# Kernel tuning notes

Hardware: AMD Instinct MI355X
Metric: run time of the kernel (lower is better)

Reference implementation:

```python
import jax, jax.numpy as jnp
import numpy as np

EPS = 1e-4
RES_BALANCE = 0.3
ATTN_BALANCE = 0.3
CLIP_ACT = 256.0
NUM_HEADS = 4
CPH = 64  # channels_per_head


def normalize(x, axes):
    # EDM2 normalize: x / (eps + ||x||_axes / sqrt(prod(axes sizes)))  -> unit RMS
    axes = tuple(axes)
    n = jnp.sqrt(jnp.sum(jnp.square(x), axis=axes, keepdims=True))
    alpha = 1.0 / np.sqrt(float(np.prod([x.shape[a] for a in axes])))
    return x / (EPS + alpha * n)


def mp_silu(x):
    return jax.nn.silu(x) / 0.596


def mp_sum(a, b, t):
    return (a + t * (b - a)) / np.sqrt((1.0 - t) ** 2 + t ** 2)


def mp_conv2d(x, w, gain=1.0):
    # MPConv: forced weight normalization per output channel, then gain/sqrt(fan_in)
    fan_in = w.shape[1] * w.shape[2] * w.shape[3]
    w = normalize(w, (1, 2, 3)) * (gain / np.sqrt(float(fan_in)))
    pad = w.shape[-1] // 2
    return jax.lax.conv_general_dilated(
        x, w, window_strides=(1, 1), padding=[(pad, pad), (pad, pad)],
        dimension_numbers=('NCHW', 'OIHW', 'NCHW'))


def mp_linear(x, w, gain=1.0):
    fan_in = w.shape[1]
    w = normalize(w, (1,)) * (gain / np.sqrt(float(fan_in)))
    return x @ w.T


def setup_inputs() -> dict:
    key = jax.random.key(0)
    ks = jax.random.split(key, 8)
    N, Cin, Cout, Cemb, H, W = 32, 256, 256, 768, 32, 32
    return {
        'x': jax.random.normal(ks[0], (N, Cin, H, W), dtype=jnp.float32),
        'emb': jax.random.normal(ks[1], (N, Cemb), dtype=jnp.float32),
        'w_res0': jax.random.normal(ks[2], (Cout, Cout, 3, 3), dtype=jnp.float32),
        'w_emb': jax.random.normal(ks[3], (Cout, Cemb), dtype=jnp.float32),
        'w_res1': jax.random.normal(ks[4], (Cout, Cout, 3, 3), dtype=jnp.float32),
        'w_qkv': jax.random.normal(ks[5], (Cout * 3, Cout, 1, 1), dtype=jnp.float32),
        'w_proj': jax.random.normal(ks[6], (Cout, Cout, 1, 1), dtype=jnp.float32),
        'emb_gain': jax.random.normal(ks[7], (), dtype=jnp.float32),
    }


def reference(x, emb, w_res0, w_emb, w_res1, w_qkv, w_proj, emb_gain):
    N, C, H, W = x.shape
    S = H * W
    # flavor == 'enc', in_channels == out_channels -> no conv_skip; resample 'keep' is identity
    x = normalize(x, (1,))  # pixel norm over channels
    y = mp_conv2d(mp_silu(x), w_res0)
    c = mp_linear(emb, w_emb, gain=emb_gain) + 1.0  # [N, C]
    y = mp_silu(y * c[:, :, None, None])
    y = mp_conv2d(y, w_res1)
    x = mp_sum(x, y, RES_BALANCE)
    # QK-normalized self-attention over H*W tokens
    y = mp_conv2d(x, w_qkv)                              # [N, 3C, H, W]
    y = y.reshape(N, NUM_HEADS, CPH, 3, S)               # channel layout (h, c, qkv)
    y = normalize(y, (2,))                               # L2-normalize per head-channel vector
    q, k, v = y[:, :, :, 0], y[:, :, :, 1], y[:, :, :, 2]  # [N, h, c, S]
    logits = jnp.einsum('nhcq,nhck->nhqk', q, k) / np.sqrt(float(CPH))
    w_att = jax.nn.softmax(logits, axis=3)
    y = jnp.einsum('nhqk,nhck->nhcq', w_att, v).reshape(N, C, H, W)
    y = mp_conv2d(y, w_proj)
    x = mp_sum(x, y, ATTN_BALANCE)
    return jnp.clip(x, -CLIP_ACT, CLIP_ACT)
```

## Files before the change

### kernel.cpp

```cpp
#include <hip/hip_runtime.h>
#include <hip/hip_bf16.h>
#include <math.h>

#define EPSV 1e-4f
#define WA 0.91914503f
#define WB 0.39392215f
#define INV596 1.6778523f

typedef __bf16 bf16x8 __attribute__((ext_vector_type(8)));
typedef short  s16x8  __attribute__((ext_vector_type(8)));
typedef float  f32x4  __attribute__((ext_vector_type(4)));
typedef _Float16 f16x8 __attribute__((ext_vector_type(8)));

__device__ inline bf16x8 bzero8() { s16x8 z = 0; return __builtin_bit_cast(bf16x8, z); }

__device__ inline void store_bf4(__hip_bfloat16* p, float a, float b, float c, float d) {
    __hip_bfloat16 t[4];
    t[0] = __float2bfloat16(a); t[1] = __float2bfloat16(b);
    t[2] = __float2bfloat16(c); t[3] = __float2bfloat16(d);
    *(short4*)p = *(short4*)t;
}

__device__ inline float bfbits2f(short u) {
    return __uint_as_float(((unsigned)(unsigned short)u) << 16);
}

__global__ __launch_bounds__(256) void wnorm_all(
        const float* __restrict__ w_res0, const float* __restrict__ w_res1,
        const float* __restrict__ w_qkv, const float* __restrict__ w_proj,
        const float* __restrict__ w_emb, const float* __restrict__ emb_gain,
        __hip_bfloat16* __restrict__ W0B, __hip_bfloat16* __restrict__ W1B,
        __hip_bfloat16* __restrict__ WQB, __hip_bfloat16* __restrict__ WPB,
        float* __restrict__ WEN) {
    __shared__ float sdata[4];
    int b = blockIdx.x;
    int tid = threadIdx.x;
    int wid = tid >> 6, lane = tid & 63;

    if (b < 512) {
        int oc = b & 255;
        const float* row = ((b < 256) ? w_res0 : w_res1) + (size_t)oc * 2304;
        __hip_bfloat16* wb = (b < 256) ? W0B : W1B;
        float ss = 0.f;
        for (int i = tid; i < 2304; i += 256) { float v = row[i]; ss += v * v; }
#pragma unroll
        for (int m = 32; m >= 1; m >>= 1) ss += __shfl_xor(ss, m);
        if (lane == 0) sdata[wid] = ss;
        __syncthreads();
        float tot = sdata[0] + sdata[1] + sdata[2] + sdata[3];
        float s = (1.0f / 48.0f) / (EPSV + sqrtf(tot) * (1.0f / 48.0f));
        for (int i = tid; i < 2304; i += 256) {
            int ic = i / 9, tap = i - ic * 9;
            wb[((size_t)tap * 256 + oc) * 256 + ic] = __float2bfloat16(row[i] * s);
        }
    } else if (b < 1536) {
        bool isq = (b < 1280);
        int oc = isq ? (b - 512) : (b - 1280);
        const float* row = (isq ? w_qkv : w_proj) + (size_t)oc * 256;
        float v0 = row[tid];
        float ss = v0 * v0;
#pragma unroll
        for (int m = 32; m >= 1; m >>= 1) ss += __shfl_xor(ss, m);
        if (lane == 0) sdata[wid] = ss;
        __syncthreads();
        float tot = sdata[0] + sdata[1] + sdata[2] + sdata[3];
        float s = 0.0625f / (EPSV + sqrtf(tot) * 0.0625f);
        if (isq) {
            int h = oc / 192, rem = oc - h * 192;
            int c = rem / 3, t = rem - c * 3;
            int newoc = t * 256 + h * 64 + c;
            WQB[(size_t)newoc * 256 + tid] = __float2bfloat16(v0 * s);
        } else {
            WPB[(size_t)oc * 256 + tid] = __float2bfloat16(v0 * s);
        }
    } else {
        int r = b - 1536;
        const float* row = w_emb + (size_t)r * 768;
        float ss = 0.f;
        for (int i = tid; i < 768; i += 256) { float v = row[i]; ss += v * v; }
#pragma unroll
        for (int m = 32; m >= 1; m >>= 1) ss += __shfl_xor(ss, m);
        if (lane == 0) sdata[wid] = ss;
        __syncthreads();
        float tot = sdata[0] + sdata[1] + sdata[2] + sdata[3];
        float g = emb_gain[0];
        float s = g * 0.036084392f / (EPSV + sqrtf(tot) * 0.036084392f);
        float* outr = WEN + (size_t)r * 768;
        for (int i = tid; i < 768; i += 256) outr[i] = row[i] * s;
    }
}

__global__ __launch_bounds__(256) void pixnorm2(const float* __restrict__ x,
        float* __restrict__ Xn, __hip_bfloat16* __restrict__ Ah) {
    int n = blockIdx.y;
    int sp = blockIdx.x * 32 + (threadIdx.x & 31);
    int cg = threadIdx.x >> 5;
    const float* xb = x + (size_t)n * 262144 + ((size_t)cg << 15) + sp;
    float v[32];
    float ss = 0.f;
#pragma unroll
    for (int i = 0; i < 32; i++) {
        v[i] = xb[(size_t)i << 10];
        ss += v[i] * v[i];
    }
    __shared__ float red[8][33];
    red[cg][threadIdx.x & 31] = ss;
    __syncthreads();
    float tot = 0.f;
#pragma unroll
    for (int j = 0; j < 8; j++) tot += red[j][threadIdx.x & 31];
    float inv = 1.0f / (EPSV + sqrtf(tot) * 0.0625f);
    float* xo = Xn + ((size_t)n * 1024 + sp) * 256 + cg * 32;
    __hip_bfloat16* ao = Ah + ((size_t)n * 1024 + sp) * 256 + cg * 32;
#pragma unroll
    for (int i = 0; i < 32; i += 4) {
        float a0 = v[i] * inv, a1 = v[i+1] * inv, a2 = v[i+2] * inv, a3 = v[i+3] * inv;
        *(float4*)&xo[i] = make_float4(a0, a1, a2, a3);
        float s0 = a0 / (1.0f + __expf(-a0)) * INV596;
        float s1 = a1 / (1.0f + __expf(-a1)) * INV596;
        float s2 = a2 / (1.0f + __expf(-a2)) * INV596;
        float s3 = a3 / (1.0f + __expf(-a3)) * INV596;
        store_bf4(&ao[i], s0, s1, s2, s3);
    }
}

__global__ void emb_kernel(const float* __restrict__ emb, const float* __restrict__ wn,
                           float* __restrict__ cvec) {
    int n = blockIdx.x;
    __shared__ float es[768];
    for (int i = threadIdx.x; i < 768; i += 256) es[i] = emb[n * 768 + i];
    __syncthreads();
    const float* wr = wn + (size_t)threadIdx.x * 768;
    float acc = 0.f;
    for (int k = 0; k < 768; k++) acc += es[k] * wr[k];
    cvec[n * 256 + threadIdx.x] = acc + 1.0f;
}

template<int KS, int ORI, int EPI, int GX>
__global__ __launch_bounds__(256) void convmfma(
        const __hip_bfloat16* __restrict__ xin,
        const __hip_bfloat16* __restrict__ wb,
        __hip_bfloat16* __restrict__ out_h,
        float* __restrict__ out_f,
        const float* __restrict__ xres,
        __hip_bfloat16* __restrict__ out_h2,
        const float* __restrict__ cvec,
        int Cin, int Cout) {
    constexpr int TAPS = KS * KS;
    constexpr int RRD = 8 + KS - 1;
    constexpr int CCD = 32 + KS - 1;
    constexpr int HLO = KS / 2;
    constexpr int NX = (RRD * 128) / 256;
    __shared__ __align__(16) __hip_bfloat16 Xl[RRD * CCD * 32];
    __shared__ __align__(16) __hip_bfloat16 Wl[TAPS * 64 * 32];

    auto xoff = [](int rr, int cc, int gran) {
        int rowl = rr * CCD + cc;
        return rowl * 32 + ((gran ^ ((rowl >> 1) & 3)) << 3);
    };
    auto woff = [](int tap, int oc, int gran) {
        int rowl = tap * 64 + oc;
        return rowl * 32 + ((gran ^ ((rowl >> 1) & 3)) << 3);
    };

    int lin = blockIdx.x + GX * (blockIdx.y + 4 * blockIdx.z);
    constexpr int NBLK = GX * 4 * 32;
    constexpr int CPX = NBLK >> 3;
    int swz = (lin & 7) * CPX + (lin >> 3);
    int oc0 = (swz % GX) * 64;
    int W = swz / GX;
    int spblk = W & 3;
    int n = W >> 2;

    int tid = threadIdx.x;
    int r0 = spblk * 8;
    int lane = tid & 63, wv = tid >> 6;
    int l15 = lane & 15, g = lane >> 4;

    if (KS == 3) {
        if (tid < RRD * 2 * 4) {
            int rr = tid >> 3;
            int side = (tid >> 2) & 1;
            int slot = tid & 3;
            *(bf16x8*)&Xl[xoff(rr, side ? (CCD - 1) : 0, slot)] = bzero8();
        }
    }

    bf16x8 xp[NX];
    bf16x8 wpf[TAPS];
    auto loadX = [&](int ch) {
#pragma unroll
        for (int u = 0; u < NX; u++) {
            int f = tid + u * 256;
            int rr = f >> 7, rem = f & 127;
            int cc = rem >> 2, slot = rem & 3;
            int gr = r0 + rr - HLO;
            bf16x8 v = bzero8();
            if ((unsigned)gr < 32u)
                v = *(const bf16x8*)&xin[((size_t)n * 1024 + gr * 32 + cc) * Cin + ch * 32 + slot * 8];
            xp[u] = v;
        }
    };
    auto writeX = [&]() {
#pragma unroll
        for (int u = 0; u < NX; u++) {
            int f = tid + u * 256;
            int rr = f >> 7, rem = f & 127;
            int cc = rem >> 2, slot = rem & 3;
            *(bf16x8*)&Xl[xoff(rr, cc + HLO, slot)] = xp[u];
        }
    };
    auto loadW = [&](int ch) {
#pragma unroll
        for (int u = 0; u < TAPS; u++) {
            int f = tid + u * 256;
            int tap = f >> 8, rem = f & 255;
            int oc = rem >> 2, slot = rem & 3;
            wpf[u] = *(const bf16x8*)&wb[((size_t)tap * Cout + oc0 + oc) * Cin + ch * 32 + slot * 8];
        }
    };
    auto writeW = [&]() {
#pragma unroll
        for (int u = 0; u < TAPS; u++) {
            int f = tid + u * 256;
            int tap = f >> 8, rem = f & 255;
            int oc = rem >> 2, slot = rem & 3;
            *(bf16x8*)&Wl[woff(tap, oc, slot)] = wpf[u];
        }
    };

    f32x4 acc[4][4];
    const f32x4 z4 = {0.f, 0.f, 0.f, 0.f};
#pragma unroll
    for (int a = 0; a < 4; a++)
#pragma unroll
        for (int b = 0; b < 4; b++) acc[a][b] = z4;

    int nch = Cin >> 5;
    loadX(0); loadW(0);
    writeX(); writeW();
    __syncthreads();

    for (int ch = 0; ch < nch; ++ch) {
        bool pf = (ch + 1 < nch);
        if (pf) { loadX(ch + 1); loadW(ch + 1); }
        if constexpr (KS == 3) {
#pragma unroll
            for (int dx = 0; dx < 3; dx++) {
                bf16x8 xv[4][2];
#pragma unroll
                for (int r = 0; r < 4; r++)
#pragma unroll
                    for (int b = 0; b < 2; b++)
                        xv[r][b] = *(const bf16x8*)&Xl[xoff(2 * wv + r, b * 16 + l15 + dx, g)];
#pragma unroll
                for (int dy = 0; dy < 3; dy++) {
                    int tap = dy * 3 + dx;
                    bf16x8 af[4];
#pragma unroll
                    for (int of = 0; of < 4; of++)
                        af[of] = *(const bf16x8*)&Wl[woff(tap, of * 16 + l15, g)];
#pragma unroll
                    for (int of = 0; of < 4; of++)
#pragma unroll
                        for (int sf = 0; sf < 4; sf++) {
                            if (ORI == 1)
                                acc[of][sf] = __builtin_amdgcn_mfma_f32_16x16x32_bf16(af[of], xv[(sf >> 1) + dy][sf & 1], acc[of][sf], 0, 0, 0);
                            else
                                acc[of][sf] = __builtin_amdgcn_mfma_f32_16x16x32_bf16(xv[(sf >> 1) + dy][sf & 1], af[of], acc[of][sf], 0, 0, 0);
                        }
                }
            }
        } else {
#pragma unroll
            for (int tap = 0; tap < TAPS; ++tap) {
                bf16x8 af[4], bfv[4];
#pragma unroll
                for (int of = 0; of < 4; of++)
                    af[of] = *(const bf16x8*)&Wl[woff(tap, of * 16 + l15, g)];
#pragma unroll
                for (int sf = 0; sf < 4; sf++) {
                    int rr = 2 * wv + (sf >> 1);
                    int cc2 = (sf & 1) * 16 + l15;
                    bfv[sf] = *(const bf16x8*)&Xl[xoff(rr, cc2, g)];
                }
#pragma unroll
                for (int of = 0; of < 4; of++)
#pragma unroll
                    for (int sf = 0; sf < 4; sf++) {
                        if (ORI == 1)
                            acc[of][sf] = __builtin_amdgcn_mfma_f32_16x16x32_bf16(af[of], bfv[sf], acc[of][sf], 0, 0, 0);
                        else
                            acc[of][sf] = __builtin_amdgcn_mfma_f32_16x16x32_bf16(bfv[sf], af[of], acc[of][sf], 0, 0, 0);
                    }
            }
        }
        __syncthreads();
        if (pf) { writeX(); writeW(); __syncthreads(); }
    }

#pragma unroll
    for (int of = 0; of < 4; of++)
#pragma unroll
        for (int sf = 0; sf < 4; sf++) {
            if constexpr (ORI == 1) {
                int row_l = 2 * wv + (sf >> 1);
                int col = (sf & 1) * 16 + l15;
                int sp = spblk * 256 + row_l * 32 + col;
                int ocb = oc0 + of * 16 + (lane >> 4) * 4;
                size_t a = ((size_t)n * 1024 + sp) * Cout + ocb;
                if constexpr (EPI == 1) {
                    float vv[4];
#pragma unroll
                    for (int r = 0; r < 4; r++) {
                        float t = acc[of][sf][r] * cvec[n * 256 + ocb + r];
                        vv[r] = t / (1.0f + __expf(-t)) * INV596;
                    }
                    store_bf4(&out_h[a], vv[0], vv[1], vv[2], vv[3]);
                } else if constexpr (EPI == 2) {
                    float4 xr = *(const float4*)&xres[a];
                    float v0 = WA * xr.x + WB * acc[of][sf][0];
                    float v1 = WA * xr.y + WB * acc[of][sf][1];
                    float v2 = WA * xr.z + WB * acc[of][sf][2];
                    float v3 = WA * xr.w + WB * acc[of][sf][3];
                    *(float4*)&out_f[a] = make_float4(v0, v1, v2, v3);
                    store_bf4(&out_h2[a], v0, v1, v2, v3);
                } else {
                    store_bf4(&out_h[a], acc[of][sf][0], acc[of][sf][1],
                              acc[of][sf][2], acc[of][sf][3]);
                }
            } else {
                int oc = oc0 + of * 16 + l15;
                int spb = spblk * 256 + (2 * wv + (sf >> 1)) * 32 + (sf & 1) * 16 + (lane >> 4) * 4;
                if constexpr (EPI == 6) {
                    float vv[4];
#pragma unroll
                    for (int r = 0; r < 4; r++) {
                        float xr = xres[((size_t)n * 1024 + spb + r) * 256 + oc];
                        float vo = WA * xr + WB * acc[of][sf][r];
                        vv[r] = fminf(fmaxf(vo, -256.f), 256.f);
                    }
                    *(float4*)&out_f[((size_t)n * 256 + oc) * 1024 + spb] =
                        make_float4(vv[0], vv[1], vv[2], vv[3]);
                }
            }
        }
}

__global__ __launch_bounds__(192) void qkvnorm3(__hip_bfloat16* __restrict__ qkv3,
                                                _Float16* __restrict__ vt) {
    int n = blockIdx.y;
    int s0 = blockIdx.x * 16;
    int tid = threadIdx.x;
    int sl = tid / 12;
    int grp = tid - sl * 12;
    int t = grp >> 2, h = grp & 3;
    __hip_bfloat16* base = qkv3 + ((size_t)(n * 1024 + s0 + sl)) * 768 + t * 256 + h * 64;
    float v[64];
    float ss = 0.f;
#pragma unroll
    for (int j = 0; j < 8; j++) {
        s16x8 b = *(const s16x8*)(base + j * 8);
#pragma unroll
        for (int e = 0; e < 8; e++) {
            float f = bfbits2f(b[e]);
            v[j * 8 + e] = f; ss += f * f;
        }
    }
    float inv = 1.0f / (EPSV + sqrtf(ss) * 0.125f);
    if (t == 0) inv *= 0.18033688f;
    __shared__ _Float16 Ts[4][64][16];
    if (t < 2) {
#pragma unroll
        for (int j = 0; j < 8; j++) {
            _Float16 tmp[8];
#pragma unroll
            for (int e = 0; e < 8; e++) tmp[e] = (_Float16)(v[j * 8 + e] * inv);
            *(s16x8*)(base + j * 8) = *(s16x8*)tmp;
        }
    } else {
#pragma unroll
        for (int c = 0; c < 64; c++) Ts[h][c][sl] = (_Float16)(v[c] * inv);
    }
    __syncthreads();
    for (int i = tid; i < 256; i += 192) {
        int hh = i >> 6, c = i & 63;
        f16x8 w0 = *(const f16x8*)&Ts[hh][c][0];
        f16x8 w1 = *(const f16x8*)&Ts[hh][c][8];
        _Float16* dst = vt + ((size_t)((n * 4 + hh) * 64 + c)) * 1024 + s0;
        *(f16x8*)dst = w0;
        *(f16x8*)(dst + 8) = w1;
    }
}

__device__ inline int swz64(int row, int c8) { return row * 64 + ((c8 ^ (row & 7)) << 3); }

__global__ __launch_bounds__(512) void attn_mfma(const _Float16* __restrict__ qkv3,
                                                 const _Float16* __restrict__ vt,
                                                 __hip_bfloat16* __restrict__ outp) {
    int lin = blockIdx.x + 4 * (blockIdx.y + 4 * blockIdx.z);
    int swz = (lin & 7) * 64 + (lin >> 3);
    int qt = swz & 3;
    int W = swz >> 2;
    int h = W & 3, n = W >> 2;

    __shared__ __align__(16) _Float16 Ks[2][64 * 64];
    __shared__ __align__(16) _Float16 Vs[2][64 * 64];
    __shared__ __align__(16) _Float16 Ps[8][32 * 64];
    int tid = threadIdx.x;
    int lane = tid & 63, wv = tid >> 6;
    int l15 = lane & 15, g = lane >> 4;

    f16x8 qreg[2][2];
#pragma unroll
    for (int nf = 0; nf < 2; nf++)
#pragma unroll
        for (int cc = 0; cc < 2; cc++)
            qreg[nf][cc] = *(const f16x8*)&qkv3[
                ((size_t)(n * 1024 + qt * 256 + wv * 32 + nf * 16 + l15)) * 768 + h * 64 + cc * 32 + g * 8];

    f16x8 kp, vp;
    int krow = tid >> 3, kslot = tid & 7;
    auto loadKV = [&](int kt) {
        kp = *(const f16x8*)&qkv3[((size_t)(n * 1024 + kt * 64 + krow)) * 768 + 256 + h * 64 + kslot * 8];
        vp = *(const f16x8*)&vt[((size_t)((n * 4 + h) * 64 + krow)) * 1024 + kt * 64 + kslot * 8];
    };
    int kdst = swz64(krow, kslot);
    auto writeKV = [&](int b) {
        *(f16x8*)&Ks[b][kdst] = kp;
        *(f16x8*)&Vs[b][kdst] = vp;
    };

    f32x4 acc_o[2][4];
    const f32x4 z4 = {0.f, 0.f, 0.f, 0.f};
#pragma unroll
    for (int a = 0; a < 2; a++)
#pragma unroll
        for (int b = 0; b < 4; b++) acc_o[a][b] = z4;
    float l_run[2] = {0.f, 0.f};

    loadKV(0); writeKV(0);
    __syncthreads();

    for (int kt = 0; kt < 16; kt++) {
        int cur = kt & 1;
        if (kt < 15) loadKV(kt + 1);

        f32x4 accs[4][2];
#pragma unroll
        for (int a = 0; a < 4; a++)
#pragma unroll
            for (int b = 0; b < 2; b++) accs[a][b] = z4;
        __builtin_amdgcn_s_setprio(1);
#pragma unroll
        for (int cc = 0; cc < 2; cc++) {
            f16x8 kf[4];
#pragma unroll
            for (int mf = 0; mf < 4; mf++)
                kf[mf] = *(const f16x8*)&Ks[cur][swz64(mf * 16 + l15, cc * 4 + g)];
#pragma unroll
            for (int mf = 0; mf < 4; mf++)
#pragma unroll
                for (int nf = 0; nf < 2; nf++)
                    accs[mf][nf] = __builtin_amdgcn_mfma_f32_16x16x32_f16(kf[mf], qreg[nf][cc], accs[mf][nf], 0, 0, 0);
        }
        __builtin_amdgcn_s_setprio(0);

#pragma unroll
        for (int nf = 0; nf < 2; nf++) {
            int q = nf * 16 + l15;
            float rs = 0.f;
#pragma unroll
            for (int mf = 0; mf < 4; mf++) {
                float p0 = __builtin_amdgcn_exp2f(accs[mf][nf][0]);
                float p1 = __builtin_amdgcn_exp2f(accs[mf][nf][1]);
                float p2 = __builtin_amdgcn_exp2f(accs[mf][nf][2]);
                float p3 = __builtin_amdgcn_exp2f(accs[mf][nf][3]);
                rs += (p0 + p1) + (p2 + p3);
                unsigned w0 = __builtin_bit_cast(unsigned, __builtin_amdgcn_cvt_pkrtz(p0, p1));
                unsigned w1 = __builtin_bit_cast(unsigned, __builtin_amdgcn_cvt_pkrtz(p2, p3));
                int elem = swz64(q, mf * 2 + (g >> 1)) + (g & 1) * 4;
                *(uint2*)&Ps[wv][elem] = make_uint2(w0, w1);
            }
            l_run[nf] += rs;
        }

        __builtin_amdgcn_s_setprio(1);
#pragma unroll
        for (int kc = 0; kc < 2; kc++) {
            f16x8 pf[2], vf[4];
#pragma unroll
            for (int mf2 = 0; mf2 < 2; mf2++)
                pf[mf2] = *(const f16x8*)&Ps[wv][swz64(mf2 * 16 + l15, kc * 4 + g)];
#pragma unroll
            for (int nf2 = 0; nf2 < 4; nf2++)
                vf[nf2] = *(const f16x8*)&Vs[cur][swz64(nf2 * 16 + l15, kc * 4 + g)];
#pragma unroll
            for (int mf2 = 0; mf2 < 2; mf2++)
#pragma unroll
                for (int nf2 = 0; nf2 < 4; nf2++)
                    acc_o[mf2][nf2] = __builtin_amdgcn_mfma_f32_16x16x32_f16(pf[mf2], vf[nf2], acc_o[mf2][nf2], 0, 0, 0);
        }
        __builtin_amdgcn_s_setprio(0);

        if (kt < 15) writeKV(cur ^ 1);
        __syncthreads();
    }

#pragma unroll
    for (int nf = 0; nf < 2; nf++) {
        float l = l_run[nf];
        l += __shfl_xor(l, 16);
        l += __shfl_xor(l, 32);
        float ilr = 1.0f / l;
#pragma unroll
        for (int r = 0; r < 4; r++) {
            float il = __shfl(ilr, g * 4 + r);
            int q = qt * 256 + wv * 32 + nf * 16 + g * 4 + r;
#pragma unroll
            for (int nf2 = 0; nf2 < 4; nf2++)
                outp[((size_t)(n * 1024 + q)) * 256 + h * 64 + nf2 * 16 + l15] =
                    __float2bfloat16(acc_o[nf][nf2][r] * il);
        }
    }
}

extern "C" void kernel_launch(void* const* d_in, const int* in_sizes, int n_in,
                              void* d_out, int out_size, void* d_ws, size_t ws_size,
                              hipStream_t stream) {
    (void)in_sizes; (void)n_in; (void)out_size; (void)ws_size;
    const float* x        = (const float*)d_in[0];
    const float* emb      = (const float*)d_in[1];
    const float* w_res0   = (const float*)d_in[2];
    const float* w_emb    = (const float*)d_in[3];
    const float* w_res1   = (const float*)d_in[4];
    const float* w_qkv    = (const float*)d_in[5];
    const float* w_proj   = (const float*)d_in[6];
    const float* emb_gain = (const float*)d_in[7];
    float* out = (float*)d_out;

    const size_t MB = 1048576;
    char* wsb = (char*)d_ws;
    float* X             = (float*)wsb;
    __hip_bfloat16* A1h  = (__hip_bfloat16*)(wsb + 32 * MB);
    __hip_bfloat16* A2h  = (__hip_bfloat16*)(wsb + 48 * MB);
    __hip_bfloat16* QKV3 = A2h;
    _Float16* Vt         = (_Float16*)d_out;
    char* wp = wsb + 96 * MB;
    __hip_bfloat16* W0B = (__hip_bfloat16*)wp;              wp += 9 * 256 * 256 * 2;
    __hip_bfloat16* W1B = (__hip_bfloat16*)wp;              wp += 9 * 256 * 256 * 2;
    __hip_bfloat16* WQB = (__hip_bfloat16*)wp;              wp += 768 * 256 * 2;
    __hip_bfloat16* WPB = (__hip_bfloat16*)wp;              wp += 256 * 256 * 2;
    float* WEN          = (float*)wp;                       wp += 256 * 768 * 4;
    float* CC           = (float*)wp;

    wnorm_all<<<1792, 256, 0, stream>>>(w_res0, w_res1, w_qkv, w_proj, w_emb, emb_gain,
                                        W0B, W1B, WQB, WPB, WEN);
    pixnorm2<<<dim3(32, 32), 256, 0, stream>>>(x, X, A1h);
    emb_kernel<<<32, 256, 0, stream>>>(emb, WEN, CC);

    convmfma<3, 1, 1, 4><<<dim3(4, 4, 32), 256, 0, stream>>>(A1h, W0B, A2h, nullptr, nullptr, nullptr, CC, 256, 256);
    convmfma<3, 1, 2, 4><<<dim3(4, 4, 32), 256, 0, stream>>>(A2h, W1B, nullptr, X, X, A1h, nullptr, 256, 256);
    convmfma<1, 1, 5, 12><<<dim3(12, 4, 32), 256, 0, stream>>>(A1h, WQB, QKV3, nullptr, nullptr, nullptr, nullptr, 256, 768);
    qkvnorm3<<<dim3(64, 32), 192, 0, stream>>>(QKV3, Vt);
    attn_mfma<<<dim3(4, 4, 32), 512, 0, stream>>>((const _Float16*)QKV3, Vt, A1h);
    convmfma<1, 2, 6, 4><<<dim3(4, 4, 32), 256, 0, stream>>>(A1h, WPB, nullptr, out, X, nullptr, nullptr, 256, 256);
}
```

Baseline: 267.9 us.

## Load conv weights directly into registers and double-buffer input tiles in LDS

Weight fragments are no longer staged through shared memory. Each wave loads its MFMA A-fragments straight from global memory into a 3-slot register ring, prefetched two taps ahead in a dx-major tap order. The input tile now uses two LDS buffers, so each channel chunk needs one barrier instead of two. This removes the LDS round trip for weights and half the synchronisation, but every wave now reads the weights redundantly from global or L2 and register pressure grows.

```diff
diff --git a/kernel.cpp b/kernel.cpp
--- a/kernel.cpp
+++ b/kernel.cpp
@@ -146,20 +146,14 @@
         __hip_bfloat16* __restrict__ out_h2,
         const float* __restrict__ cvec,
         int Cin, int Cout) {
-    constexpr int TAPS = KS * KS;
     constexpr int RRD = 8 + KS - 1;
     constexpr int CCD = 32 + KS - 1;
     constexpr int HLO = KS / 2;
     constexpr int NX = (RRD * 128) / 256;
-    __shared__ __align__(16) __hip_bfloat16 Xl[RRD * CCD * 32];
-    __shared__ __align__(16) __hip_bfloat16 Wl[TAPS * 64 * 32];
+    __shared__ __align__(16) __hip_bfloat16 Xl[2][RRD * CCD * 32];
 
     auto xoff = [](int rr, int cc, int gran) {
         int rowl = rr * CCD + cc;
-        return rowl * 32 + ((gran ^ ((rowl >> 1) & 3)) << 3);
-    };
-    auto woff = [](int tap, int oc, int gran) {
-        int rowl = tap * 64 + oc;
         return rowl * 32 + ((gran ^ ((rowl >> 1) & 3)) << 3);
     };
 
@@ -182,12 +176,12 @@
             int rr = tid >> 3;
             int side = (tid >> 2) & 1;
             int slot = tid & 3;
-            *(bf16x8*)&Xl[xoff(rr, side ? (CCD - 1) : 0, slot)] = bzero8();
+            *(bf16x8*)&Xl[0][xoff(rr, side ? (CCD - 1) : 0, slot)] = bzero8();
+            *(bf16x8*)&Xl[1][xoff(rr, side ? (CCD - 1) : 0, slot)] = bzero8();
         }
     }
 
     bf16x8 xp[NX];
-    bf16x8 wpf[TAPS];
     auto loadX = [&](int ch) {
 #pragma unroll
         for (int u = 0; u < NX; u++) {
@@ -201,32 +195,22 @@
             xp[u] = v;
         }
     };
-    auto writeX = [&]() {
+    auto writeX = [&](int buf) {
 #pragma unroll
         for (int u = 0; u < NX; u++) {
             int f = tid + u * 256;
             int rr = f >> 7, rem = f & 127;
             int cc = rem >> 2, slot = rem & 3;
-            *(bf16x8*)&Xl[xoff(rr, cc + HLO, slot)] = xp[u];
+            *(bf16x8*)&Xl[buf][xoff(rr, cc + HLO, slot)] = xp[u];
         }
     };
-    auto loadW = [&](int ch) {
-#pragma unroll
-        for (int u = 0; u < TAPS; u++) {
-            int f = tid + u * 256;
-            int tap = f >> 8, rem = f & 255;
-            int oc = rem >> 2, slot = rem & 3;
-            wpf[u] = *(const bf16x8*)&wb[((size_t)tap * Cout + oc0 + oc) * Cin + ch * 32 + slot * 8];
-        }
-    };
-    auto writeW = [&]() {
-#pragma unroll
-        for (int u = 0; u < TAPS; u++) {
-            int f = tid + u * 256;
-            int tap = f >> 8, rem = f & 255;
-            int oc = rem >> 2, slot = rem & 3;
-            *(bf16x8*)&Wl[woff(tap, oc, slot)] = wpf[u];
-        }
+
+    bf16x8 afr[3][4];
+    auto issueW = [&](int slot, int ch, int tap) {
+#pragma unroll
+        for (int of = 0; of < 4; of++)
+            afr[slot][of] = *(const bf16x8*)&wb[
+                ((size_t)(tap * Cout + oc0 + of * 16 + l15)) * Cin + ch * 32 + g * 8];
     };
 
     f32x4 acc[4][4];
@@ -237,53 +221,60 @@
         for (int b = 0; b < 4; b++) acc[a][b] = z4;
 
     int nch = Cin >> 5;
-    loadX(0); loadW(0);
-    writeX(); writeW();
+    constexpr int ORD3[9] = {0, 3, 6, 1, 4, 7, 2, 5, 8};
+
+    loadX(0);
+    writeX(0);
+    if constexpr (KS == 3) { issueW(0, 0, ORD3[0]); issueW(1, 0, ORD3[1]); }
+    else                   { issueW(0, 0, 0); issueW(1, 1, 0); }
     __syncthreads();
 
-    for (int ch = 0; ch < nch; ++ch) {
-        bool pf = (ch + 1 < nch);
-        if (pf) { loadX(ch + 1); loadW(ch + 1); }
-        if constexpr (KS == 3) {
-#pragma unroll
-            for (int dx = 0; dx < 3; dx++) {
-                bf16x8 xv[4][2];
-#pragma unroll
-                for (int r = 0; r < 4; r++)
+    int cur = 0;
+    if constexpr (KS == 3) {
+        for (int ch = 0; ch < nch; ++ch) {
+            bool pf = (ch + 1 < nch);
+            if (pf) loadX(ch + 1);
+#pragma unroll
+            for (int u = 0; u < 9; u++) {
+                const int dy = u % 3, dx = u / 3;
+                bf16x8 af[4];
+#pragma unroll
+                for (int of = 0; of < 4; of++) af[of] = afr[u % 3][of];
+                const int nx = u + 2;
+                if (nx < 9) issueW((u + 2) % 3, ch, ORD3[nx]);
+                else if (pf) issueW((u + 2) % 3, ch + 1, ORD3[nx - 9]);
+                bf16x8 xv[2][2];
+#pragma unroll
+                for (int r = 0; r < 2; r++)
 #pragma unroll
                     for (int b = 0; b < 2; b++)
-                        xv[r][b] = *(const bf16x8*)&Xl[xoff(2 * wv + r, b * 16 + l15 + dx, g)];
-#pragma unroll
-                for (int dy = 0; dy < 3; dy++) {
-                    int tap = dy * 3 + dx;
-                    bf16x8 af[4];
-#pragma unroll
-                    for (int of = 0; of < 4; of++)
-                        af[of] = *(const bf16x8*)&Wl[woff(tap, of * 16 + l15, g)];
-#pragma unroll
-                    for (int of = 0; of < 4; of++)
-#pragma unroll
-                        for (int sf = 0; sf < 4; sf++) {
-                            if (ORI == 1)
-                                acc[of][sf] = __builtin_amdgcn_mfma_f32_16x16x32_bf16(af[of], xv[(sf >> 1) + dy][sf & 1], acc[of][sf], 0, 0, 0);
-                            else
-                                acc[of][sf] = __builtin_amdgcn_mfma_f32_16x16x32_bf16(xv[(sf >> 1) + dy][sf & 1], af[of], acc[of][sf], 0, 0, 0);
-                        }
-                }
+                        xv[r][b] = *(const bf16x8*)&Xl[cur][xoff(2 * wv + r + dy, b * 16 + l15 + dx, g)];
+#pragma unroll
+                for (int of = 0; of < 4; of++)
+#pragma unroll
+                    for (int sf = 0; sf < 4; sf++) {
+                        if (ORI == 1)
+                            acc[of][sf] = __builtin_amdgcn_mfma_f32_16x16x32_bf16(af[of], xv[sf >> 1][sf & 1], acc[of][sf], 0, 0, 0);
+                        else
+                            acc[of][sf] = __builtin_amdgcn_mfma_f32_16x16x32_bf16(xv[sf >> 1][sf & 1], af[of], acc[of][sf], 0, 0, 0);
+                    }
             }
-        } else {
-#pragma unroll
-            for (int tap = 0; tap < TAPS; ++tap) {
-                bf16x8 af[4], bfv[4];
-#pragma unroll
-                for (int of = 0; of < 4; of++)
-                    af[of] = *(const bf16x8*)&Wl[woff(tap, of * 16 + l15, g)];
-#pragma unroll
-                for (int sf = 0; sf < 4; sf++) {
-                    int rr = 2 * wv + (sf >> 1);
-                    int cc2 = (sf & 1) * 16 + l15;
-                    bfv[sf] = *(const bf16x8*)&Xl[xoff(rr, cc2, g)];
-                }
+            if (pf) writeX(cur ^ 1);
+            __syncthreads();
+            cur ^= 1;
+        }
+    } else {
+        for (int ch = 0; ch < nch; ch += 2) {
+            loadX(ch + 1);
+            {
+                bf16x8 af[4];
+#pragma unroll
+                for (int of = 0; of < 4; of++) af[of] = afr[0][of];
+                if (ch + 2 < nch) issueW(0, ch + 2, 0);
+                bf16x8 bfv[4];
+#pragma unroll
+                for (int sf = 0; sf < 4; sf++)
+                    bfv[sf] = *(const bf16x8*)&Xl[cur][xoff(2 * wv + (sf >> 1), (sf & 1) * 16 + l15, g)];
 #pragma unroll
                 for (int of = 0; of < 4; of++)
 #pragma unroll
@@ -294,9 +285,34 @@
                             acc[of][sf] = __builtin_amdgcn_mfma_f32_16x16x32_bf16(bfv[sf], af[of], acc[of][sf], 0, 0, 0);
                     }
             }
-        }
-        __syncthreads();
-        if (pf) { writeX(); writeW(); __syncthreads(); }
+            writeX(cur ^ 1);
+            __syncthreads();
+            cur ^= 1;
+            bool pf1 = (ch + 2 < nch);
+            if (pf1) loadX(ch + 2);
+            {
+                bf16x8 af[4];
+#pragma unroll
+                for (int of = 0; of < 4; of++) af[of] = afr[1][of];
+                if (ch + 3 < nch) issueW(1, ch + 3, 0);
+                bf16x8 bfv[4];
+#pragma unroll
+                for (int sf = 0; sf < 4; sf++)
+                    bfv[sf] = *(const bf16x8*)&Xl[cur][xoff(2 * wv + (sf >> 1), (sf & 1) * 16 + l15, g)];
+#pragma unroll
+                for (int of = 0; of < 4; of++)
+#pragma unroll
+                    for (int sf = 0; sf < 4; sf++) {
+                        if (ORI == 1)
+                            acc[of][sf] = __builtin_amdgcn_mfma_f32_16x16x32_bf16(af[of], bfv[sf], acc[of][sf], 0, 0, 0);
+                        else
+                            acc[of][sf] = __builtin_amdgcn_mfma_f32_16x16x32_bf16(bfv[sf], af[of], acc[of][sf], 0, 0, 0);
+                    }
+            }
+            if (pf1) writeX(cur ^ 1);
+            __syncthreads();
+            cur ^= 1;
+        }
     }
 
 #pragma unroll
```

After: 391.4 us. +46.1%, slower.

## Fuse QKV normalization into QKV conv epilogue and merge prep kernels

Applied to the files above, without the earlier changes.

Folds per-head L2 normalization of q/k/v into the 1x1 QKV conv epilogue. The conv now writes fp16 q/k and a transposed fp16 v directly, so the separate qkvnorm pass and its bf16 round-trip through global memory go away. Weight normalization, the embedding matvec and the pixel norm are merged into one prep launch, which removes two launches and the intermediate normalized-embedding buffer. The transposed v stores from the epilogue are scalar and strided, which may be less coalesced than the old shared-memory transpose.

```diff
diff --git a/kernel.cpp b/kernel.cpp
--- a/kernel.cpp
+++ b/kernel.cpp
@@ -21,17 +21,21 @@
     *(short4*)p = *(short4*)t;
 }
 
-__device__ inline float bfbits2f(short u) {
-    return __uint_as_float(((unsigned)(unsigned short)u) << 16);
+__device__ inline void store_f16x4(_Float16* p, float a, float b, float c, float d) {
+    _Float16 t[4];
+    t[0] = (_Float16)a; t[1] = (_Float16)b; t[2] = (_Float16)c; t[3] = (_Float16)d;
+    *(uint2*)p = *(uint2*)t;
 }
 
-__global__ __launch_bounds__(256) void wnorm_all(
+__global__ __launch_bounds__(256) void prep_all(
+        const float* __restrict__ x, const float* __restrict__ emb,
         const float* __restrict__ w_res0, const float* __restrict__ w_res1,
         const float* __restrict__ w_qkv, const float* __restrict__ w_proj,
         const float* __restrict__ w_emb, const float* __restrict__ emb_gain,
         __hip_bfloat16* __restrict__ W0B, __hip_bfloat16* __restrict__ W1B,
         __hip_bfloat16* __restrict__ WQB, __hip_bfloat16* __restrict__ WPB,
-        float* __restrict__ WEN) {
+        float* __restrict__ CC, float* __restrict__ Xn,
+        __hip_bfloat16* __restrict__ Ah) {
     __shared__ float sdata[4];
     int b = blockIdx.x;
     int tid = threadIdx.x;
@@ -73,7 +77,7 @@
         } else {
             WPB[(size_t)oc * 256 + tid] = __float2bfloat16(v0 * s);
         }
-    } else {
+    } else if (b < 1792) {
         int r = b - 1536;
         const float* row = w_emb + (size_t)r * 768;
         float ss = 0.f;
@@ -85,55 +89,49 @@
         float tot = sdata[0] + sdata[1] + sdata[2] + sdata[3];
         float g = emb_gain[0];
         float s = g * 0.036084392f / (EPSV + sqrtf(tot) * 0.036084392f);
-        float* outr = WEN + (size_t)r * 768;
-        for (int i = tid; i < 768; i += 256) outr[i] = row[i] * s;
+        __shared__ float rowS[768];
+        for (int i = tid; i < 768; i += 256) rowS[i] = row[i] * s;
+        __syncthreads();
+        int n_ = tid >> 3, k0 = tid & 7;
+        float p = 0.f;
+        for (int k = k0; k < 768; k += 8) p += emb[n_ * 768 + k] * rowS[k];
+        p += __shfl_xor(p, 1);
+        p += __shfl_xor(p, 2);
+        p += __shfl_xor(p, 4);
+        if (k0 == 0) CC[n_ * 256 + r] = p + 1.0f;
+    } else {
+        int idx = b - 1792;
+        int n = idx >> 5;
+        int sp = (idx & 31) * 32 + (tid & 31);
+        int cg = tid >> 5;
+        const float* xb = x + (size_t)n * 262144 + ((size_t)cg << 15) + sp;
+        float v[32];
+        float ss = 0.f;
+#pragma unroll
+        for (int i = 0; i < 32; i++) {
+            v[i] = xb[(size_t)i << 10];
+            ss += v[i] * v[i];
+        }
+        __shared__ float red[8][33];
+        red[cg][tid & 31] = ss;
+        __syncthreads();
+        float tot = 0.f;
+#pragma unroll
+        for (int j = 0; j < 8; j++) tot += red[j][tid & 31];
+        float inv = 1.0f / (EPSV + sqrtf(tot) * 0.0625f);
+        float* xo = Xn + ((size_t)n * 1024 + sp) * 256 + cg * 32;
+        __hip_bfloat16* ao = Ah + ((size_t)n * 1024 + sp) * 256 + cg * 32;
+#pragma unroll
+        for (int i = 0; i < 32; i += 4) {
+            float a0 = v[i] * inv, a1 = v[i+1] * inv, a2 = v[i+2] * inv, a3 = v[i+3] * inv;
+            *(float4*)&xo[i] = make_float4(a0, a1, a2, a3);
+            float s0 = a0 / (1.0f + __expf(-a0)) * INV596;
+            float s1 = a1 / (1.0f + __expf(-a1)) * INV596;
+            float s2 = a2 / (1.0f + __expf(-a2)) * INV596;
+            float s3 = a3 / (1.0f + __expf(-a3)) * INV596;
+            store_bf4(&ao[i], s0, s1, s2, s3);
+        }
     }
-}
-
-__global__ __launch_bounds__(256) void pixnorm2(const float* __restrict__ x,
-        float* __restrict__ Xn, __hip_bfloat16* __restrict__ Ah) {
-    int n = blockIdx.y;
-    int sp = blockIdx.x * 32 + (threadIdx.x & 31);
-    int cg = threadIdx.x >> 5;
-    const float* xb = x + (size_t)n * 262144 + ((size_t)cg << 15) + sp;
-    float v[32];
-    float ss = 0.f;
-#pragma unroll
-    for (int i = 0; i < 32; i++) {
-        v[i] = xb[(size_t)i << 10];
-        ss += v[i] * v[i];
-    }
-    __shared__ float red[8][33];
-    red[cg][threadIdx.x & 31] = ss;
-    __syncthreads();
-    float tot = 0.f;
-#pragma unroll
-    for (int j = 0; j < 8; j++) tot += red[j][threadIdx.x & 31];
-    float inv = 1.0f / (EPSV + sqrtf(tot) * 0.0625f);
-    float* xo = Xn + ((size_t)n * 1024 + sp) * 256 + cg * 32;
-    __hip_bfloat16* ao = Ah + ((size_t)n * 1024 + sp) * 256 + cg * 32;
-#pragma unroll
-    for (int i = 0; i < 32; i += 4) {
-        float a0 = v[i] * inv, a1 = v[i+1] * inv, a2 = v[i+2] * inv, a3 = v[i+3] * inv;
-        *(float4*)&xo[i] = make_float4(a0, a1, a2, a3);
-        float s0 = a0 / (1.0f + __expf(-a0)) * INV596;
-        float s1 = a1 / (1.0f + __expf(-a1)) * INV596;
-        float s2 = a2 / (1.0f + __expf(-a2)) * INV596;
-        float s3 = a3 / (1.0f + __expf(-a3)) * INV596;
-        store_bf4(&ao[i], s0, s1, s2, s3);
-    }
-}
-
-__global__ void emb_kernel(const float* __restrict__ emb, const float* __restrict__ wn,
-                           float* __restrict__ cvec) {
-    int n = blockIdx.x;
-    __shared__ float es[768];
-    for (int i = threadIdx.x; i < 768; i += 256) es[i] = emb[n * 768 + i];
-    __syncthreads();
-    const float* wr = wn + (size_t)threadIdx.x * 768;
-    float acc = 0.f;
-    for (int k = 0; k < 768; k++) acc += es[k] * wr[k];
-    cvec[n * 256 + threadIdx.x] = acc + 1.0f;
 }
 
 template<int KS, int ORI, int EPI, int GX>
@@ -143,7 +141,7 @@
         __hip_bfloat16* __restrict__ out_h,
         float* __restrict__ out_f,
         const float* __restrict__ xres,
-        __hip_bfloat16* __restrict__ out_h2,
+        _Float16* __restrict__ vt_out,
         const float* __restrict__ cvec,
         int Cin, int Cout) {
     constexpr int TAPS = KS * KS;
@@ -299,6 +297,44 @@
         if (pf) { writeX(); writeW(); __syncthreads(); }
     }
 
+    if constexpr (EPI == 7) {
+        int t_ = oc0 >> 8;
+        int h_ = (oc0 >> 6) & 3;
+        _Float16* qk16 = (_Float16*)out_h;
+#pragma unroll
+        for (int sf = 0; sf < 4; sf++) {
+            int sp = spblk * 256 + (2 * wv + (sf >> 1)) * 32 + (sf & 1) * 16 + l15;
+            float ss = 0.f;
+#pragma unroll
+            for (int of = 0; of < 4; of++)
+#pragma unroll
+                for (int r = 0; r < 4; r++) ss += acc[of][sf][r] * acc[of][sf][r];
+            ss += __shfl_xor(ss, 16);
+            ss += __shfl_xor(ss, 32);
+            float inv = 1.0f / (EPSV + sqrtf(ss) * 0.125f);
+            if (t_ == 0) inv *= 0.18033688f;
+            if (t_ < 2) {
+#pragma unroll
+                for (int of = 0; of < 4; of++) {
+                    int ocb = oc0 + of * 16 + g * 4;
+                    store_f16x4(&qk16[((size_t)n * 1024 + sp) * 768 + ocb],
+                                acc[of][sf][0] * inv, acc[of][sf][1] * inv,
+                                acc[of][sf][2] * inv, acc[of][sf][3] * inv);
+                }
+            } else {
+#pragma unroll
+                for (int of = 0; of < 4; of++)
+#pragma unroll
+                    for (int r = 0; r < 4; r++) {
+                        int c = (of * 16 + g * 4 + r) & 63;
+                        vt_out[((size_t)((n * 4 + h_) * 64 + c)) * 1024 + sp] =
+                            (_Float16)(acc[of][sf][r] * inv);
+                    }
+            }
+        }
+        return;
+    }
+
 #pragma unroll
     for (int of = 0; of < 4; of++)
 #pragma unroll
@@ -307,7 +343,7 @@
                 int row_l = 2 * wv + (sf >> 1);
                 int col = (sf & 1) * 16 + l15;
                 int sp = spblk * 256 + row_l * 32 + col;
-                int ocb = oc0 + of * 16 + (lane >> 4) * 4;
+                int ocb = oc0 + of * 16 + g * 4;
                 size_t a = ((size_t)n * 1024 + sp) * Cout + ocb;
                 if constexpr (EPI == 1) {
                     float vv[4];
@@ -324,14 +360,11 @@
                     float v2 = WA * xr.z + WB * acc[of][sf][2];
                     float v3 = WA * xr.w + WB * acc[of][sf][3];
                     *(float4*)&out_f[a] = make_float4(v0, v1, v2, v3);
-                    store_bf4(&out_h2[a], v0, v1, v2, v3);
-                } else {
-                    store_bf4(&out_h[a], acc[of][sf][0], acc[of][sf][1],
-                              acc[of][sf][2], acc[of][sf][3]);
+                    store_bf4(&out_h[a], v0, v1, v2, v3);
                 }
             } else {
                 int oc = oc0 + of * 16 + l15;
-                int spb = spblk * 256 + (2 * wv + (sf >> 1)) * 32 + (sf & 1) * 16 + (lane >> 4) * 4;
+                int spb = spblk * 256 + (2 * wv + (sf >> 1)) * 32 + (sf & 1) * 16 + g * 4;
                 if constexpr (EPI == 6) {
                     float vv[4];
 #pragma unroll
@@ -345,52 +378,6 @@
                 }
             }
         }
-}
-
-__global__ __launch_bounds__(192) void qkvnorm3(__hip_bfloat16* __restrict__ qkv3,
-                                                _Float16* __restrict__ vt) {
-    int n = blockIdx.y;
-    int s0 = blockIdx.x * 16;
-    int tid = threadIdx.x;
-    int sl = tid / 12;
-    int grp = tid - sl * 12;
-    int t = grp >> 2, h = grp & 3;
-    __hip_bfloat16* base = qkv3 + ((size_t)(n * 1024 + s0 + sl)) * 768 + t * 256 + h * 64;
-    float v[64];
-    float ss = 0.f;
-#pragma unroll
-    for (int j = 0; j < 8; j++) {
-        s16x8 b = *(const s16x8*)(base + j * 8);
-#pragma unroll
-        for (int e = 0; e < 8; e++) {
-            float f = bfbits2f(b[e]);
-            v[j * 8 + e] = f; ss += f * f;
-        }
-    }
-    float inv = 1.0f / (EPSV + sqrtf(ss) * 0.125f);
-    if (t == 0) inv *= 0.18033688f;
-    __shared__ _Float16 Ts[4][64][16];
-    if (t < 2) {
-#pragma unroll
-        for (int j = 0; j < 8; j++) {
-            _Float16 tmp[8];
-#pragma unroll
-            for (int e = 0; e < 8; e++) tmp[e] = (_Float16)(v[j * 8 + e] * inv);
-            *(s16x8*)(base + j * 8) = *(s16x8*)tmp;
-        }
-    } else {
-#pragma unroll
-        for (int c = 0; c < 64; c++) Ts[h][c][sl] = (_Float16)(v[c] * inv);
-    }
-    __syncthreads();
-    for (int i = tid; i < 256; i += 192) {
-        int hh = i >> 6, c = i & 63;
-        f16x8 w0 = *(const f16x8*)&Ts[hh][c][0];
-        f16x8 w1 = *(const f16x8*)&Ts[hh][c][8];
-        _Float16* dst = vt + ((size_t)((n * 4 + hh) * 64 + c)) * 1024 + s0;
-        *(f16x8*)dst = w0;
-        *(f16x8*)(dst + 8) = w1;
-    }
 }
 
 __device__ inline int swz64(int row, int c8) { return row * 64 + ((c8 ^ (row & 7)) << 3); }
@@ -551,18 +538,14 @@
     __hip_bfloat16* W1B = (__hip_bfloat16*)wp;              wp += 9 * 256 * 256 * 2;
     __hip_bfloat16* WQB = (__hip_bfloat16*)wp;              wp += 768 * 256 * 2;
     __hip_bfloat16* WPB = (__hip_bfloat16*)wp;              wp += 256 * 256 * 2;
-    float* WEN          = (float*)wp;                       wp += 256 * 768 * 4;
     float* CC           = (float*)wp;
 
-    wnorm_all<<<1792, 256, 0, stream>>>(w_res0, w_res1, w_qkv, w_proj, w_emb, emb_gain,
-                                        W0B, W1B, WQB, WPB, WEN);
-    pixnorm2<<<dim3(32, 32), 256, 0, stream>>>(x, X, A1h);
-    emb_kernel<<<32, 256, 0, stream>>>(emb, WEN, CC);
+    prep_all<<<2816, 256, 0, stream>>>(x, emb, w_res0, w_res1, w_qkv, w_proj, w_emb,
+                                       emb_gain, W0B, W1B, WQB, WPB, CC, X, A1h);
 
     convmfma<3, 1, 1, 4><<<dim3(4, 4, 32), 256, 0, stream>>>(A1h, W0B, A2h, nullptr, nullptr, nullptr, CC, 256, 256);
-    convmfma<3, 1, 2, 4><<<dim3(4, 4, 32), 256, 0, stream>>>(A2h, W1B, nullptr, X, X, A1h, nullptr, 256, 256);
-    convmfma<1, 1, 5, 12><<<dim3(12, 4, 32), 256, 0, stream>>>(A1h, WQB, QKV3, nullptr, nullptr, nullptr, nullptr, 256, 768);
-    qkvnorm3<<<dim3(64, 32), 192, 0, stream>>>(QKV3, Vt);
+    convmfma<3, 1, 2, 4><<<dim3(4, 4, 32), 256, 0, stream>>>(A2h, W1B, A1h, X, X, nullptr, nullptr, 256, 256);
+    convmfma<1, 1, 7, 12><<<dim3(12, 4, 32), 256, 0, stream>>>(A1h, WQB, QKV3, nullptr, nullptr, Vt, nullptr, 256, 768);
     attn_mfma<<<dim3(4, 4, 32), 512, 0, stream>>>((const _Float16*)QKV3, Vt, A1h);
     convmfma<1, 2, 6, 4><<<dim3(4, 4, 32), 256, 0, stream>>>(A1h, WPB, nullptr, out, X, nullptr, nullptr, 256, 256);
 }
```

New measurement: 219.1 us, median of 2. 18.2% less time.
